# Kernel optimization log

Hardware: AMD Instinct MI355X
Metric: run time of the kernel (lower is better)

## Reference

```python
import jax, jax.numpy as jnp
import numpy as np
from jax.scipy.special import logsumexp

S = 4          # num_residual_streams
D = 1024       # dim
B, T = 2, 4096
SINKHORN_ITERS = 10
TAU = 0.05


def rmsnorm(x, gamma):
    # F.normalize(x, dim=-1) * sqrt(dim) * (gamma + 1)
    norm = jnp.sqrt(jnp.sum(x * x, axis=-1, keepdims=True))
    scale = jnp.asarray(x.shape[-1], x.dtype) ** 0.5
    return x / jnp.maximum(norm, 1e-12) * scale * (gamma + 1.0)


def sinkhorn_log(logits, num_iters=SINKHORN_ITERS, tau=TAU):
    Z = logits / tau                      # (..., n, n)
    u = jnp.zeros(Z.shape[:-1], Z.dtype)  # (..., n)
    v = jnp.zeros_like(u)
    for _ in range(num_iters):
        u = -logsumexp(Z + v[..., None, :], axis=-1)
        v = -logsumexp(Z + u[..., :, None], axis=-2)
    return jnp.exp(Z + u[..., :, None] + v[..., None, :])


def setup_inputs() -> dict:
    key = jax.random.key(0)
    ks = jax.random.split(key, 8)
    residuals = jax.random.normal(ks[0], (B, T, S, D), dtype=jnp.float32)
    gamma = jnp.zeros((S * D,), dtype=jnp.float32)             # RMSNorm gamma init
    w_res = 0.02 * jax.random.normal(ks[1], (S * S, S * D), dtype=jnp.float32)
    w_pre = 0.02 * jax.random.normal(ks[2], (S, S * D), dtype=jnp.float32)
    w_post = 0.02 * jax.random.normal(ks[3], (S, S * D), dtype=jnp.float32)
    beta_res = jnp.full((S, S), -8.0, dtype=jnp.float32).at[jnp.arange(S), jnp.arange(S)].set(0.0)
    beta_pre = jnp.full((S,), -8.0, dtype=jnp.float32).at[0].set(0.0)  # layer_index=0
    beta_post = jnp.zeros((S,), dtype=jnp.float32)
    alpha_res = jnp.asarray(0.01, dtype=jnp.float32)
    alpha_pre = jnp.asarray(0.01, dtype=jnp.float32)
    alpha_post = jnp.asarray(0.01, dtype=jnp.float32)
    return dict(residuals=residuals, gamma=gamma, w_res=w_res, w_pre=w_pre,
                w_post=w_post, beta_res=beta_res, beta_pre=beta_pre,
                beta_post=beta_post, alpha_res=alpha_res, alpha_pre=alpha_pre,
                alpha_post=alpha_post)


def reference(residuals, gamma, w_res, w_pre, w_post, beta_res, beta_pre,
              beta_post, alpha_res, alpha_pre, alpha_post):
    b, t, s, d = residuals.shape
    h = residuals.reshape(b, t, s * d)
    normed = rmsnorm(h, gamma)                                  # (b,t,s*d)
    # dynamic H logits: static beta + alpha * linear(normed)
    res_logits = beta_res + alpha_res * jnp.einsum('btk,ek->bte', normed, w_res).reshape(b, t, s, s)
    H_res = sinkhorn_log(res_logits)                            # (b,t,s,s) doubly stochastic
    H_pre = jax.nn.softmax(beta_pre + alpha_pre * jnp.einsum('btk,sk->bts', normed, w_pre), axis=-1)
    H_post = 2.0 * jax.nn.sigmoid(beta_post + alpha_post * jnp.einsum('btk,sk->bts', normed, w_post))
    branch_in = jnp.einsum('bts,btsd->btd', H_pre, residuals)   # stream pooling -> branch input
    branch_out = branch_in                                      # identity branch
    mixed = jnp.einsum('btij,btjd->btid', H_res, residuals)     # stream remixing
    out = mixed + H_post[..., None] * branch_out[:, :, None, :]
    return out
```

## Files before the change

kernel.cpp:

```cpp
#include <hip/hip_runtime.h>
#include <math.h>

#define TOK_PER_BLK 2
#define THREADS 256
#define NROWS 24
#define PCOL 68
#define TAU_INV 20.0f
#define WCOPY 8
#define WROW_U32 2048
#define WCOPY_U32 (NROWS * WROW_U32)

typedef _Float16 half2_t __attribute__((ext_vector_type(2)));
typedef float    f32x4  __attribute__((ext_vector_type(4)));

__global__ void fold_gamma(const float* __restrict__ w_res,
                           const float* __restrict__ w_pre,
                           const float* __restrict__ w_post,
                           const float* __restrict__ gamma,
                           unsigned int* __restrict__ wf) {
    const int idx = blockIdx.x * THREADS + threadIdx.x;
    const int row = idx >> 11;
    const int j   = idx & 2047;
    const int o   = j >> 2;
    const int pp  = j & 3;
    const int t   = o & 255;
    const int quad = pp >> 1;
    int base;
    if (o < 256) base = (quad == 0) ? (4 * t)        : (1024 + 4 * t);
    else         base = (quad == 0) ? (2048 + 4 * t) : (3072 + 4 * t);
    const int k0 = base + 2 * (pp & 1);

    const float* src = (row < 16) ? (w_res + ((size_t)row << 12))
                     : (row < 20) ? (w_pre + ((size_t)(row - 16) << 12))
                                  : (w_post + ((size_t)(row - 20) << 12));
    float v0 = src[k0]     * (1.0f + gamma[k0]);
    float v1 = src[k0 + 1] * (1.0f + gamma[k0 + 1]);
    union { _Float16 h[2]; unsigned int u; } cvt;
    cvt.h[0] = (_Float16)v0;
    cvt.h[1] = (_Float16)v1;
    #pragma unroll
    for (int c = 0; c < WCOPY; ++c)
        wf[(size_t)c * WCOPY_U32 + idx] = cvt.u;
}

__global__ __launch_bounds__(THREADS, 2)
void hc_fused(const float* __restrict__ resid,
              const unsigned int* __restrict__ wf,
              const float* __restrict__ beta_res,
              const float* __restrict__ beta_pre,
              const float* __restrict__ beta_post,
              const float* __restrict__ p_alpha_res,
              const float* __restrict__ p_alpha_pre,
              const float* __restrict__ p_alpha_post,
              float* __restrict__ out)
{
    __shared__ __align__(16) float sh_part[NROWS * TOK_PER_BLK][PCOL];
    __shared__ __align__(16) float sh_ssqp[TOK_PER_BLK][PCOL];
    __shared__ float sh_raw[TOK_PER_BLK][NROWS];
    __shared__ float sh_ssq[TOK_PER_BLK];
    __shared__ float sh_M[TOK_PER_BLK][16];

    const int tid  = threadIdx.x;
    const int wave = tid >> 6;
    const int lane = tid & 63;
    const long tok0 = (long)blockIdx.x * TOK_PER_BLK;

    const f32x4* hp = (const f32x4*)resid + tok0 * 1024;
    half2_t xh[TOK_PER_BLK][8];
    #pragma unroll
    for (int m = 0; m < TOK_PER_BLK; ++m) {
        f32x4 pf[4];
        #pragma unroll
        for (int q = 0; q < 4; ++q)
            pf[q] = __builtin_nontemporal_load(&hp[m * 1024 + q * 256 + tid]);
        float s = 0.f;
        #pragma unroll
        for (int q = 0; q < 4; ++q) {
            f32x4 v = pf[q];
            s += v.x * v.x + v.y * v.y + v.z * v.z + v.w * v.w;
            xh[m][2 * q]     = half2_t{(_Float16)v.x, (_Float16)v.y};
            xh[m][2 * q + 1] = half2_t{(_Float16)v.z, (_Float16)v.w};
        }
        s += __shfl_xor(s, 16, 64);
        s += __shfl_xor(s, 32, 64);
        if (lane < 16) sh_ssqp[m][wave * 16 + lane] = s;
    }

    const uint4* wp = (const uint4*)(wf + (size_t)(blockIdx.x & (WCOPY - 1)) * WCOPY_U32);

    auto load_row = [&](int e, uint4 (&w)[2]) {
        const uint4* wr = wp + ((size_t)e << 9);
        w[0] = wr[tid];
        w[1] = wr[256 + tid];
    };
#define H2(u) __builtin_bit_cast(half2_t, (u))
    auto comp_row = [&](int e, const uint4 (&W)[2]) {
        #pragma unroll
        for (int m = 0; m < TOK_PER_BLK; ++m) {
            float a = 0.f;
            a = __builtin_amdgcn_fdot2(H2(W[0].x), xh[m][0], a, false);
            a = __builtin_amdgcn_fdot2(H2(W[0].y), xh[m][1], a, false);
            a = __builtin_amdgcn_fdot2(H2(W[0].z), xh[m][2], a, false);
            a = __builtin_amdgcn_fdot2(H2(W[0].w), xh[m][3], a, false);
            a = __builtin_amdgcn_fdot2(H2(W[1].x), xh[m][4], a, false);
            a = __builtin_amdgcn_fdot2(H2(W[1].y), xh[m][5], a, false);
            a = __builtin_amdgcn_fdot2(H2(W[1].z), xh[m][6], a, false);
            a = __builtin_amdgcn_fdot2(H2(W[1].w), xh[m][7], a, false);
            a += __shfl_xor(a, 16, 64);
            a += __shfl_xor(a, 32, 64);
            if (lane < 16) sh_part[e * TOK_PER_BLK + m][wave * 16 + lane] = a;
        }
    };
#undef H2

    uint4 wA[2], wB[2], wC[2], wD[2];
    load_row(0, wA);
    load_row(1, wB);
    load_row(2, wC);
    load_row(3, wD);
    #pragma unroll 1
    for (int c = 0; c < 6; ++c) {
        comp_row(4 * c + 0, wA);
        if (4 * c + 4 < NROWS) load_row(4 * c + 4, wA);
        comp_row(4 * c + 1, wB);
        if (4 * c + 5 < NROWS) load_row(4 * c + 5, wB);
        comp_row(4 * c + 2, wC);
        if (4 * c + 6 < NROWS) load_row(4 * c + 6, wC);
        comp_row(4 * c + 3, wD);
        if (4 * c + 7 < NROWS) load_row(4 * c + 7, wD);
    }
    __syncthreads();

    if (tid < NROWS * TOK_PER_BLK) {
        const float4* src = (const float4*)&sh_part[tid][0];
        float4 s4 = src[0];
        #pragma unroll
        for (int j = 1; j < 16; ++j) {
            float4 v = src[j];
            s4.x += v.x; s4.y += v.y; s4.z += v.z; s4.w += v.w;
        }
        sh_raw[tid & (TOK_PER_BLK - 1)][tid >> 1] = s4.x + s4.y + s4.z + s4.w;
    } else if (tid < NROWS * TOK_PER_BLK + TOK_PER_BLK) {
        const int m = tid - NROWS * TOK_PER_BLK;
        const float4* src = (const float4*)&sh_ssqp[m][0];
        float4 s4 = src[0];
        #pragma unroll
        for (int j = 1; j < 16; ++j) {
            float4 v = src[j];
            s4.x += v.x; s4.y += v.y; s4.z += v.z; s4.w += v.w;
        }
        sh_ssq[m] = s4.x + s4.y + s4.z + s4.w;
    }
    __syncthreads();

    if (wave < TOK_PER_BLK) {
        const int m   = wave;
        const int idx = lane & 15;
        const int jj  = idx & 3;

        float ss    = sh_ssq[m];
        float scale = 64.0f / fmaxf(sqrtf(ss), 1e-12f);

        const float a_res  = p_alpha_res[0];
        const float a_pre  = p_alpha_pre[0];
        const float a_post = p_alpha_post[0];

        float Z = (beta_res[idx] + a_res * scale * sh_raw[m][idx]) * TAU_INV;
        float u = 0.f, v = 0.f;
        #pragma unroll 1
        for (int it = 0; it < 10; ++it) {
            float tv = Z + v;
            float mx = tv;
            mx = fmaxf(mx, __shfl_xor(mx, 1, 64));
            mx = fmaxf(mx, __shfl_xor(mx, 2, 64));
            float sm = __expf(tv - mx);
            sm += __shfl_xor(sm, 1, 64);
            sm += __shfl_xor(sm, 2, 64);
            u = -(mx + __logf(sm));
            tv = Z + u;
            mx = tv;
            mx = fmaxf(mx, __shfl_xor(mx, 4, 64));
            mx = fmaxf(mx, __shfl_xor(mx, 8, 64));
            sm = __expf(tv - mx);
            sm += __shfl_xor(sm, 4, 64);
            sm += __shfl_xor(sm, 8, 64);
            v = -(mx + __logf(sm));
        }
        float P = __expf(Z + u + v);

        float lpre = beta_pre[jj] + a_pre * scale * sh_raw[m][16 + jj];
        float mxp = lpre;
        mxp = fmaxf(mxp, __shfl_xor(mxp, 1, 64));
        mxp = fmaxf(mxp, __shfl_xor(mxp, 2, 64));
        float ep = __expf(lpre - mxp);
        float sp = ep;
        sp += __shfl_xor(sp, 1, 64);
        sp += __shfl_xor(sp, 2, 64);
        float hpre = ep / sp;
        float lpost = beta_post[jj] + a_post * scale * sh_raw[m][20 + jj];
        float hpost = 2.0f / (1.0f + __expf(-lpost));

        float hpost_i = __shfl(hpost, idx >> 2, 64);
        float Mv = P + hpost_i * hpre;
        if (lane < 16) sh_M[m][idx] = Mv;
    }
    __syncthreads();

    #pragma unroll
    for (int m = 0; m < TOK_PER_BLK; ++m) {
        float Mv[16];
        #pragma unroll
        for (int k = 0; k < 16; ++k) Mv[k] = sh_M[m][k];

        float xm[16];
        #pragma unroll
        for (int q = 0; q < 4; ++q) {
            xm[4*q + 0] = (float)xh[m][2*q][0];
            xm[4*q + 1] = (float)xh[m][2*q][1];
            xm[4*q + 2] = (float)xh[m][2*q + 1][0];
            xm[4*q + 3] = (float)xh[m][2*q + 1][1];
        }

        f32x4* op = (f32x4*)out + (tok0 + m) * 1024;
        #pragma unroll
        for (int i = 0; i < 4; ++i) {
            f32x4 o;
            o.x = Mv[i*4+0]*xm[0] + Mv[i*4+1]*xm[4]  + Mv[i*4+2]*xm[8]  + Mv[i*4+3]*xm[12];
            o.y = Mv[i*4+0]*xm[1] + Mv[i*4+1]*xm[5]  + Mv[i*4+2]*xm[9]  + Mv[i*4+3]*xm[13];
            o.z = Mv[i*4+0]*xm[2] + Mv[i*4+1]*xm[6]  + Mv[i*4+2]*xm[10] + Mv[i*4+3]*xm[14];
            o.w = Mv[i*4+0]*xm[3] + Mv[i*4+1]*xm[7]  + Mv[i*4+2]*xm[11] + Mv[i*4+3]*xm[15];
            __builtin_nontemporal_store(o, &op[i * 256 + tid]);
        }
    }
}

extern "C" void kernel_launch(void* const* d_in, const int* in_sizes, int n_in,
                              void* d_out, int out_size, void* d_ws, size_t ws_size,
                              hipStream_t stream) {
    const float* resid      = (const float*)d_in[0];
    const float* gamma      = (const float*)d_in[1];
    const float* w_res      = (const float*)d_in[2];
    const float* w_pre      = (const float*)d_in[3];
    const float* w_post     = (const float*)d_in[4];
    const float* beta_res   = (const float*)d_in[5];
    const float* beta_pre   = (const float*)d_in[6];
    const float* beta_post  = (const float*)d_in[7];
    const float* alpha_res  = (const float*)d_in[8];
    const float* alpha_pre  = (const float*)d_in[9];
    const float* alpha_post = (const float*)d_in[10];
    float* out = (float*)d_out;

    unsigned int* wf = (unsigned int*)d_ws;
    (void)ws_size;

    fold_gamma<<<NROWS * 2048 / THREADS, THREADS, 0, stream>>>(
        w_res, w_pre, w_post, gamma, wf);

    const int ntok = in_sizes[0] / 4096;
    const int grid = ntok / TOK_PER_BLK;

    hc_fused<<<grid, THREADS, 0, stream>>>(resid, wf, beta_res, beta_pre,
                                           beta_post, alpha_res, alpha_pre,
                                           alpha_post, out);
}
```

Before: 277.0 us.

## Process four tokens per block and reduce partials with adjacent-lane shuffles

Doubles tokens per block from two to four so each weight row loaded from global memory is reused across more tokens, halving weight traffic per token. The intra-wave reduction now combines adjacent lanes (xor 1,2) instead of distant lanes (xor 16,32), and the dot products are split into two independent accumulators for more instruction-level parallelism. All four waves now run the Sinkhorn epilogue, one token each. The cost is higher register pressure from holding four tokens' fp16 inputs, which could lower occupancy, and the reduction index mapping changes, which has to match the fold_gamma weight layout.

```diff
diff --git a/kernel.cpp b/kernel.cpp
--- a/kernel.cpp
+++ b/kernel.cpp
@@ -1,7 +1,7 @@
 #include <hip/hip_runtime.h>
 #include <math.h>
 
-#define TOK_PER_BLK 2
+#define TOK_PER_BLK 4
 #define THREADS 256
 #define NROWS 24
 #define PCOL 68
@@ -81,9 +81,9 @@
             xh[m][2 * q]     = half2_t{(_Float16)v.x, (_Float16)v.y};
             xh[m][2 * q + 1] = half2_t{(_Float16)v.z, (_Float16)v.w};
         }
-        s += __shfl_xor(s, 16, 64);
-        s += __shfl_xor(s, 32, 64);
-        if (lane < 16) sh_ssqp[m][wave * 16 + lane] = s;
+        s += __shfl_xor(s, 1, 64);
+        s += __shfl_xor(s, 2, 64);
+        if ((lane & 3) == 0) sh_ssqp[m][wave * 16 + (lane >> 2)] = s;
     }
 
     const uint4* wp = (const uint4*)(wf + (size_t)(blockIdx.x & (WCOPY - 1)) * WCOPY_U32);
@@ -97,18 +97,20 @@
     auto comp_row = [&](int e, const uint4 (&W)[2]) {
         #pragma unroll
         for (int m = 0; m < TOK_PER_BLK; ++m) {
-            float a = 0.f;
-            a = __builtin_amdgcn_fdot2(H2(W[0].x), xh[m][0], a, false);
-            a = __builtin_amdgcn_fdot2(H2(W[0].y), xh[m][1], a, false);
-            a = __builtin_amdgcn_fdot2(H2(W[0].z), xh[m][2], a, false);
-            a = __builtin_amdgcn_fdot2(H2(W[0].w), xh[m][3], a, false);
-            a = __builtin_amdgcn_fdot2(H2(W[1].x), xh[m][4], a, false);
-            a = __builtin_amdgcn_fdot2(H2(W[1].y), xh[m][5], a, false);
-            a = __builtin_amdgcn_fdot2(H2(W[1].z), xh[m][6], a, false);
-            a = __builtin_amdgcn_fdot2(H2(W[1].w), xh[m][7], a, false);
-            a += __shfl_xor(a, 16, 64);
-            a += __shfl_xor(a, 32, 64);
-            if (lane < 16) sh_part[e * TOK_PER_BLK + m][wave * 16 + lane] = a;
+            float a0 = 0.f, a1 = 0.f;
+            a0 = __builtin_amdgcn_fdot2(H2(W[0].x), xh[m][0], a0, false);
+            a0 = __builtin_amdgcn_fdot2(H2(W[0].y), xh[m][1], a0, false);
+            a0 = __builtin_amdgcn_fdot2(H2(W[0].z), xh[m][2], a0, false);
+            a0 = __builtin_amdgcn_fdot2(H2(W[0].w), xh[m][3], a0, false);
+            a1 = __builtin_amdgcn_fdot2(H2(W[1].x), xh[m][4], a1, false);
+            a1 = __builtin_amdgcn_fdot2(H2(W[1].y), xh[m][5], a1, false);
+            a1 = __builtin_amdgcn_fdot2(H2(W[1].z), xh[m][6], a1, false);
+            a1 = __builtin_amdgcn_fdot2(H2(W[1].w), xh[m][7], a1, false);
+            float a = a0 + a1;
+            a += __shfl_xor(a, 1, 64);
+            a += __shfl_xor(a, 2, 64);
+            if ((lane & 3) == 0)
+                sh_part[e * TOK_PER_BLK + m][wave * 16 + (lane >> 2)] = a;
         }
     };
 #undef H2
@@ -132,14 +134,15 @@
     __syncthreads();
 
     if (tid < NROWS * TOK_PER_BLK) {
-        const float4* src = (const float4*)&sh_part[tid][0];
+        const int e = tid >> 2, m = tid & 3;
+        const float4* src = (const float4*)&sh_part[e * TOK_PER_BLK + m][0];
         float4 s4 = src[0];
         #pragma unroll
         for (int j = 1; j < 16; ++j) {
             float4 v = src[j];
             s4.x += v.x; s4.y += v.y; s4.z += v.z; s4.w += v.w;
         }
-        sh_raw[tid & (TOK_PER_BLK - 1)][tid >> 1] = s4.x + s4.y + s4.z + s4.w;
+        sh_raw[m][e] = s4.x + s4.y + s4.z + s4.w;
     } else if (tid < NROWS * TOK_PER_BLK + TOK_PER_BLK) {
         const int m = tid - NROWS * TOK_PER_BLK;
         const float4* src = (const float4*)&sh_ssqp[m][0];
@@ -153,7 +156,7 @@
     }
     __syncthreads();
 
-    if (wave < TOK_PER_BLK) {
+    {
         const int m   = wave;
         const int idx = lane & 15;
         const int jj  = idx & 3;
```

Measured after the change: 287.6 us. 3.8% more time.
